# Performance work log

Hardware: AMD Instinct MI355X
Metric: run time of the kernel (lower is better)

The kernel has to match this reference:

```python
import jax, jax.numpy as jnp
import numpy as np

M, K, N = 8192, 4096, 11008
GS = 128
G = K // GS  # 32 groups along reduction dim


def setup_inputs() -> dict:
    key = jax.random.key(0)
    k1, k2, k3, k4 = jax.random.split(key, 4)
    inp = jax.random.normal(k1, (M, K), dtype=jnp.float32)
    # packed int4 weights: two nibbles per byte along K -> [K//2, N]
    weight = jax.random.randint(k2, (K // 2, N), 0, 256, dtype=jnp.int32)
    scale = jax.random.uniform(k3, (G, N), dtype=jnp.float32)
    zp = jax.random.randint(k4, (G, N), 0, 16, dtype=jnp.int32)
    return {"input": inp, "weight": weight, "scale": scale, "zp": zp, "gs": GS}


def dequant_int4(weight, scale, zp, gs):
    # unpack nibbles: low nibble first, then high -> interleaved along K
    low = weight & 0xF            # [K//2, N]
    high = (weight >> 4) & 0xF    # [K//2, N]
    w = jnp.stack([low, high], axis=1).reshape(weight.shape[0] * 2, weight.shape[1])  # [K, N]
    g = w.shape[0] // gs
    wg = w.reshape(g, gs, w.shape[1])                          # [G, gs, N]
    wd = (wg - zp[:, None, :]).astype(scale.dtype) * scale[:, None, :]
    return wd.reshape(w.shape[0], w.shape[1])                  # [K, N] float


def reference(input, weight, scale, zp, gs):
    W = dequant_int4(weight, scale, zp, gs)      # [K, N]
    return input @ W                             # [M, N]
```

## Files before the change

### kernel.cpp

```cpp
#include <hip/hip_runtime.h>


constexpr int M = 8192;
constexpr int K = 4096;
constexpr int N = 11008;

constexpr int BM = 128;
constexpr int BN = 128;
constexpr int BK = 64;

typedef short v8s __attribute__((ext_vector_type(8)));
typedef float v4f __attribute__((ext_vector_type(4)));

__device__ __forceinline__ unsigned pack_bf16(float lo, float hi) {
    unsigned a = __builtin_bit_cast(unsigned, lo);
    a += 0x7FFFu + ((a >> 16) & 1u);
    unsigned b = __builtin_bit_cast(unsigned, hi);
    b += 0x7FFFu + ((b >> 16) & 1u);
    return (a >> 16) | (b & 0xFFFF0000u);
}

__global__ __launch_bounds__(256) void tile_a(const float* __restrict__ A,
                                              uint4* __restrict__ At)
{
    const size_t u = (size_t)blockIdx.x * 256 + threadIdx.x;
    const int r  = (int)(u & 127);
    const int c  = (int)((u >> 7) & 7);
    const int kt = (int)((u >> 10) & 63);
    const int mt = (int)(u >> 16);
    const float* src = A + (size_t)(mt * 128 + r) * K + kt * 64 + c * 8;
    float4 f0 = *reinterpret_cast<const float4*>(src);
    float4 f1 = *reinterpret_cast<const float4*>(src + 4);
    uint4 w;
    w.x = pack_bf16(f0.x, f0.y);
    w.y = pack_bf16(f0.z, f0.w);
    w.z = pack_bf16(f1.x, f1.y);
    w.w = pack_bf16(f1.z, f1.w);
    At[u] = w;
}

__global__ __launch_bounds__(256) void tile_b(const int* __restrict__ Wq,
                                              const float* __restrict__ scale,
                                              const int* __restrict__ zp,
                                              uint4* __restrict__ Bt)
{
    const size_t u = (size_t)blockIdx.x * 256 + threadIdx.x;
    const int r  = (int)(u & 127);
    const int c  = (int)((u >> 7) & 7);
    const int kt = (int)((u >> 10) & 63);
    const int nt = (int)(u >> 16);
    const int n  = nt * 128 + r;
    const int g  = kt >> 1;
    const float sc = scale[(size_t)g * N + n];
    const float zs = -sc * (float)zp[(size_t)g * N + n];
    const int* src = Wq + (size_t)(kt * 32 + c * 4) * N + n;
    unsigned q0 = (unsigned)src[0];
    unsigned q1 = (unsigned)src[(size_t)N];
    unsigned q2 = (unsigned)src[(size_t)2 * N];
    unsigned q3 = (unsigned)src[(size_t)3 * N];
    uint4 o;
    o.x = pack_bf16(fmaf((float)(q0 & 15u), sc, zs),
                    fmaf((float)((q0 >> 4) & 15u), sc, zs));
    o.y = pack_bf16(fmaf((float)(q1 & 15u), sc, zs),
                    fmaf((float)((q1 >> 4) & 15u), sc, zs));
    o.z = pack_bf16(fmaf((float)(q2 & 15u), sc, zs),
                    fmaf((float)((q2 >> 4) & 15u), sc, zs));
    o.w = pack_bf16(fmaf((float)(q3 & 15u), sc, zs),
                    fmaf((float)((q3 >> 4) & 15u), sc, zs));
    Bt[u] = o;
}

__global__ __launch_bounds__(256) void qgemm_bf16(
    const unsigned short* __restrict__ At,
    const unsigned short* __restrict__ Bt,
    float* __restrict__ C)
{
    __shared__ unsigned short sA[(BK / 8) * BM * 8];
    __shared__ unsigned short sB[(BK / 8) * BN * 8];

    const int t = threadIdx.x;

    const int lane = t & 63;
    const int wave = t >> 6;
    const int wm   = (wave & 1) * 64;
    const int wn   = (wave >> 1) * 64;
    const int l16  = lane & 15;
    const int quad = lane >> 4;

    v4f acc[4][4];
    #pragma unroll
    for (int i = 0; i < 4; ++i)
        #pragma unroll
        for (int j = 0; j < 4; ++j)
            acc[i][j] = (v4f){0.f, 0.f, 0.f, 0.f};

    for (int kt = 0; kt < K / BK; ++kt) {
        const unsigned short* aTile = At + ((size_t)(blockIdx.x * 64 + kt) * 1024) * 8;
        const unsigned short* bTile = Bt + ((size_t)(blockIdx.y * 64 + kt) * 1024) * 8;

        __syncthreads();

        #pragma unroll
        for (int i = 0; i < 4; ++i) {
            const int s = i * 256 + t;
            const unsigned short* ga = aTile + (size_t)s * 8;
            const unsigned short* gb = bTile + (size_t)s * 8;
            unsigned short* la = sA + (size_t)(s & ~63) * 8;
            unsigned short* lb = sB + (size_t)(s & ~63) * 8;
            __builtin_amdgcn_global_load_lds(
                (const __attribute__((address_space(1))) void*)ga,
                (__attribute__((address_space(3))) void*)la, 16, 0, 0);
            __builtin_amdgcn_global_load_lds(
                (const __attribute__((address_space(1))) void*)gb,
                (__attribute__((address_space(3))) void*)lb, 16, 0, 0);
        }

        asm volatile("s_waitcnt vmcnt(0)" ::: "memory");
        __syncthreads();

        #pragma unroll
        for (int kw = 0; kw < 2; ++kw) {
            const int cb = kw * 4 + quad;
            v8s af[4], bfr[4];
            #pragma unroll
            for (int i = 0; i < 4; ++i)
                af[i] = *reinterpret_cast<const v8s*>(
                    &sA[(cb * BM + wm + i * 16 + l16) * 8]);
            #pragma unroll
            for (int j = 0; j < 4; ++j)
                bfr[j] = *reinterpret_cast<const v8s*>(
                    &sB[(cb * BN + wn + j * 16 + l16) * 8]);
            #pragma unroll
            for (int i = 0; i < 4; ++i)
                #pragma unroll
                for (int j = 0; j < 4; ++j)
                    acc[i][j] = __builtin_amdgcn_mfma_f32_16x16x32_bf16(
                        af[i], bfr[j], acc[i][j], 0, 0, 0);
        }
    }

    const int m0 = blockIdx.x * BM;
    const int n0 = blockIdx.y * BN;
    #pragma unroll
    for (int i = 0; i < 4; ++i) {
        int rbase = m0 + wm + i * 16 + quad * 4;
        #pragma unroll
        for (int j = 0; j < 4; ++j) {
            int col = n0 + wn + j * 16 + l16;
            #pragma unroll
            for (int r = 0; r < 4; ++r)
                C[(size_t)(rbase + r) * N + col] = acc[i][j][r];
        }
    }
}

__global__ __launch_bounds__(256) void qgemm_kernel(
    const float* __restrict__ A,
    const int*   __restrict__ Wq,
    const float* __restrict__ scale,
    const int*   __restrict__ zp,
    float*       __restrict__ C)
{
    __shared__ unsigned short sA[(BK / 8) * BM * 8];
    __shared__ unsigned short sB[(BK / 8) * BN * 8];

    const int t  = threadIdx.x;
    const int m0 = blockIdx.x * BM;
    const int n0 = blockIdx.y * BN;

    const int lane = t & 63;
    const int wave = t >> 6;
    const int wm   = (wave & 1) * 64;
    const int wn   = (wave >> 1) * 64;
    const int l16  = lane & 15;
    const int quad = lane >> 4;

    const int bn  = t & 127;
    const int brg = t >> 7;

    v4f acc[4][4];
    #pragma unroll
    for (int i = 0; i < 4; ++i)
        #pragma unroll
        for (int j = 0; j < 4; ++j)
            acc[i][j] = (v4f){0.f, 0.f, 0.f, 0.f};

    for (int kt = 0; kt < K / BK; ++kt) {
        const int k0 = kt * BK;
        const int gq = k0 >> 7;
        const float sc = scale[gq * N + n0 + bn];
        const float zs = -sc * (float)zp[gq * N + n0 + bn];

        __syncthreads();

        #pragma unroll
        for (int p = 0; p < 4; ++p) {
            int idx = t + p * 256;
            int m = idx >> 3;
            int c = idx & 7;
            const float* src = A + (size_t)(m0 + m) * K + k0 + c * 8;
            float4 f0 = *reinterpret_cast<const float4*>(src);
            float4 f1 = *reinterpret_cast<const float4*>(src + 4);
            uint4 w;
            w.x = pack_bf16(f0.x, f0.y);
            w.y = pack_bf16(f0.z, f0.w);
            w.z = pack_bf16(f1.x, f1.y);
            w.w = pack_bf16(f1.z, f1.w);
            *reinterpret_cast<uint4*>(&sA[(c * BM + m) * 8]) = w;
        }

        #pragma unroll
        for (int p = 0; p < 4; ++p) {
            int g = brg + p * 2;
            const int* src = Wq + (size_t)((k0 >> 1) + g * 4) * N + n0 + bn;
            unsigned q0 = (unsigned)src[0];
            unsigned q1 = (unsigned)src[N];
            unsigned q2 = (unsigned)src[2 * N];
            unsigned q3 = (unsigned)src[3 * N];
            uint4 o;
            o.x = pack_bf16(fmaf((float)(q0 & 15u), sc, zs),
                            fmaf((float)((q0 >> 4) & 15u), sc, zs));
            o.y = pack_bf16(fmaf((float)(q1 & 15u), sc, zs),
                            fmaf((float)((q1 >> 4) & 15u), sc, zs));
            o.z = pack_bf16(fmaf((float)(q2 & 15u), sc, zs),
                            fmaf((float)((q2 >> 4) & 15u), sc, zs));
            o.w = pack_bf16(fmaf((float)(q3 & 15u), sc, zs),
                            fmaf((float)((q3 >> 4) & 15u), sc, zs));
            *reinterpret_cast<uint4*>(&sB[(g * BN + bn) * 8]) = o;
        }

        __syncthreads();

        #pragma unroll
        for (int kw = 0; kw < 2; ++kw) {
            int cb = kw * 4 + quad;
            v8s af[4], bfr[4];
            #pragma unroll
            for (int i = 0; i < 4; ++i)
                af[i] = *reinterpret_cast<const v8s*>(&sA[(cb * BM + wm + i * 16 + l16) * 8]);
            #pragma unroll
            for (int j = 0; j < 4; ++j)
                bfr[j] = *reinterpret_cast<const v8s*>(&sB[(cb * BN + wn + j * 16 + l16) * 8]);
            #pragma unroll
            for (int i = 0; i < 4; ++i)
                #pragma unroll
                for (int j = 0; j < 4; ++j)
                    acc[i][j] = __builtin_amdgcn_mfma_f32_16x16x32_bf16(
                        af[i], bfr[j], acc[i][j], 0, 0, 0);
        }
    }

    #pragma unroll
    for (int i = 0; i < 4; ++i) {
        int rbase = m0 + wm + i * 16 + quad * 4;
        #pragma unroll
        for (int j = 0; j < 4; ++j) {
            int col = n0 + wn + j * 16 + l16;
            #pragma unroll
            for (int r = 0; r < 4; ++r)
                C[(size_t)(rbase + r) * N + col] = acc[i][j][r];
        }
    }
}

extern "C" void kernel_launch(void* const* d_in, const int* in_sizes, int n_in,
                              void* d_out, int out_size, void* d_ws, size_t ws_size,
                              hipStream_t stream) {
    const float* A     = (const float*)d_in[0];
    const int*   Wq    = (const int*)d_in[1];
    const float* scale = (const float*)d_in[2];
    const int*   zp    = (const int*)d_in[3];
    float*       C     = (float*)d_out;

    const size_t needA = (size_t)M * K * 2;
    const size_t needB = (size_t)(N / 128) * (K / 64) * 1024 * 16;

    if (d_ws != nullptr && ws_size >= needA + needB) {
        unsigned short* At = (unsigned short*)d_ws;
        unsigned short* Bt = (unsigned short*)((char*)d_ws + needA);

        tile_a<<<dim3((unsigned)((size_t)M * K / 8 / 256)), dim3(256), 0, stream>>>(
            A, (uint4*)At);
        tile_b<<<dim3((unsigned)((size_t)(N / 128) * (K / 64) * 1024 / 256)), dim3(256), 0,
                 stream>>>(Wq, scale, zp, (uint4*)Bt);
        qgemm_bf16<<<dim3(M / BM, N / BN), dim3(256), 0, stream>>>(At, Bt, C);
    } else {
        qgemm_kernel<<<dim3(M / BM, N / BN), dim3(256), 0, stream>>>(A, Wq, scale, zp, C);
    }
}
```

Before: 1.268 ms.

## Fuse prep kernels and use 256x256 tiles with 4-stage LDS pipeline

Merges the A-conversion and B-dequant tiling kernels into a single prep launch, rearranged for 256-wide tiles with BK=32. The bf16 GEMM now uses 512-thread blocks computing 256x256 tiles. It keeps three global_load_lds stages in flight across a 4-buffer LDS ring, using partial vmcnt waits, and raises wave priority around the MFMA block. The aim is to hide global-load latency behind compute and raise arithmetic intensity per tile. In exchange it needs 128KB of LDS per block, which limits occupancy to one block per CU, and a larger accumulator register footprint.

```diff
diff --git a/kernel.cpp b/kernel.cpp
--- a/kernel.cpp
+++ b/kernel.cpp
@@ -5,9 +5,10 @@
 constexpr int K = 4096;
 constexpr int N = 11008;
 
-constexpr int BM = 128;
-constexpr int BN = 128;
-constexpr int BK = 64;
+constexpr int BM = 256;
+constexpr int BN = 256;
+constexpr int BK = 32;
+constexpr int KT = K / BK;
 
 typedef short v8s __attribute__((ext_vector_type(8)));
 typedef float v4f __attribute__((ext_vector_type(4)));
@@ -20,65 +21,184 @@
     return (a >> 16) | (b & 0xFFFF0000u);
 }
 
-__global__ __launch_bounds__(256) void tile_a(const float* __restrict__ A,
-                                              uint4* __restrict__ At)
-{
-    const size_t u = (size_t)blockIdx.x * 256 + threadIdx.x;
-    const int r  = (int)(u & 127);
-    const int c  = (int)((u >> 7) & 7);
-    const int kt = (int)((u >> 10) & 63);
-    const int mt = (int)(u >> 16);
-    const float* src = A + (size_t)(mt * 128 + r) * K + kt * 64 + c * 8;
-    float4 f0 = *reinterpret_cast<const float4*>(src);
-    float4 f1 = *reinterpret_cast<const float4*>(src + 4);
-    uint4 w;
-    w.x = pack_bf16(f0.x, f0.y);
-    w.y = pack_bf16(f0.z, f0.w);
-    w.z = pack_bf16(f1.x, f1.y);
-    w.w = pack_bf16(f1.z, f1.w);
-    At[u] = w;
-}
-
-__global__ __launch_bounds__(256) void tile_b(const int* __restrict__ Wq,
-                                              const float* __restrict__ scale,
-                                              const int* __restrict__ zp,
-                                              uint4* __restrict__ Bt)
-{
-    const size_t u = (size_t)blockIdx.x * 256 + threadIdx.x;
-    const int r  = (int)(u & 127);
-    const int c  = (int)((u >> 7) & 7);
-    const int kt = (int)((u >> 10) & 63);
-    const int nt = (int)(u >> 16);
-    const int n  = nt * 128 + r;
-    const int g  = kt >> 1;
-    const float sc = scale[(size_t)g * N + n];
-    const float zs = -sc * (float)zp[(size_t)g * N + n];
-    const int* src = Wq + (size_t)(kt * 32 + c * 4) * N + n;
-    unsigned q0 = (unsigned)src[0];
-    unsigned q1 = (unsigned)src[(size_t)N];
-    unsigned q2 = (unsigned)src[(size_t)2 * N];
-    unsigned q3 = (unsigned)src[(size_t)3 * N];
-    uint4 o;
-    o.x = pack_bf16(fmaf((float)(q0 & 15u), sc, zs),
-                    fmaf((float)((q0 >> 4) & 15u), sc, zs));
-    o.y = pack_bf16(fmaf((float)(q1 & 15u), sc, zs),
-                    fmaf((float)((q1 >> 4) & 15u), sc, zs));
-    o.z = pack_bf16(fmaf((float)(q2 & 15u), sc, zs),
-                    fmaf((float)((q2 >> 4) & 15u), sc, zs));
-    o.w = pack_bf16(fmaf((float)(q3 & 15u), sc, zs),
-                    fmaf((float)((q3 >> 4) & 15u), sc, zs));
-    Bt[u] = o;
-}
-
-__global__ __launch_bounds__(256) void qgemm_bf16(
+constexpr int PREP_A_BLOCKS = (M / 256) * KT * 256 / 256;
+constexpr int PREP_B_BLOCKS = (N / 256) * KT * 4 * 256 / 256;
+
+__global__ __launch_bounds__(256) void prep(const float* __restrict__ A,
+                                            const int* __restrict__ Wq,
+                                            const float* __restrict__ scale,
+                                            const int* __restrict__ zp,
+                                            uint4* __restrict__ At,
+                                            uint4* __restrict__ Bt)
+{
+    const int tid = threadIdx.x;
+    if (blockIdx.x < PREP_A_BLOCKS) {
+        const int u  = blockIdx.x * 256 + tid;
+        const int r  = u & 255;
+        const int kt = (u >> 8) & 127;
+        const int mt = u >> 15;
+        const float* src = A + (size_t)(mt * 256 + r) * K + kt * 32;
+        float4 f[8];
+        #pragma unroll
+        for (int i = 0; i < 8; ++i)
+            f[i] = reinterpret_cast<const float4*>(src)[i];
+        const size_t base = (size_t)(mt * KT + kt) * 1024 + r;
+        #pragma unroll
+        for (int c = 0; c < 4; ++c) {
+            uint4 w;
+            w.x = pack_bf16(f[2 * c].x, f[2 * c].y);
+            w.y = pack_bf16(f[2 * c].z, f[2 * c].w);
+            w.z = pack_bf16(f[2 * c + 1].x, f[2 * c + 1].y);
+            w.w = pack_bf16(f[2 * c + 1].z, f[2 * c + 1].w);
+            At[base + c * 256] = w;
+        }
+    } else {
+        const size_t u = (size_t)(blockIdx.x - PREP_A_BLOCKS) * 256 + tid;
+        const int r  = (int)(u & 255);
+        const int c  = (int)((u >> 8) & 3);
+        const int kt = (int)((u >> 10) & 127);
+        const int nt = (int)(u >> 17);
+        const int n  = nt * 256 + r;
+        const int g  = kt >> 2;
+        const float sc = scale[(size_t)g * N + n];
+        const float zs = -sc * (float)zp[(size_t)g * N + n];
+        const int* src = Wq + (size_t)(kt * 16 + c * 4) * N + n;
+        unsigned q0 = (unsigned)src[0];
+        unsigned q1 = (unsigned)src[(size_t)N];
+        unsigned q2 = (unsigned)src[(size_t)2 * N];
+        unsigned q3 = (unsigned)src[(size_t)3 * N];
+        uint4 o;
+        o.x = pack_bf16(fmaf((float)(q0 & 15u), sc, zs),
+                        fmaf((float)((q0 >> 4) & 15u), sc, zs));
+        o.y = pack_bf16(fmaf((float)(q1 & 15u), sc, zs),
+                        fmaf((float)((q1 >> 4) & 15u), sc, zs));
+        o.z = pack_bf16(fmaf((float)(q2 & 15u), sc, zs),
+                        fmaf((float)((q2 >> 4) & 15u), sc, zs));
+        o.w = pack_bf16(fmaf((float)(q3 & 15u), sc, zs),
+                        fmaf((float)((q3 >> 4) & 15u), sc, zs));
+        Bt[u] = o;
+    }
+}
+
+
+__device__ __forceinline__ void stage_step(const unsigned short* __restrict__ At,
+                                           const unsigned short* __restrict__ Bt,
+                                           int bx, int by, int t, int buf,
+                                           int tid, unsigned short* sMem)
+{
+    const unsigned short* aT = At + (size_t)(bx * KT + t) * 1024 * 8;
+    const unsigned short* bT = Bt + (size_t)(by * KT + t) * 1024 * 8;
+    unsigned short* sa = sMem + (size_t)buf * 2048 * 8;
+    unsigned short* sb = sa + 1024 * 8;
+    #pragma unroll
+    for (int i = 0; i < 2; ++i) {
+        const int s = i * 512 + tid;
+        __builtin_amdgcn_global_load_lds(
+            (const __attribute__((address_space(1))) void*)(aT + (size_t)s * 8),
+            (__attribute__((address_space(3))) void*)(sa + (size_t)(s & ~63) * 8),
+            16, 0, 0);
+        __builtin_amdgcn_global_load_lds(
+            (const __attribute__((address_space(1))) void*)(bT + (size_t)s * 8),
+            (__attribute__((address_space(3))) void*)(sb + (size_t)(s & ~63) * 8),
+            16, 0, 0);
+    }
+}
+
+__device__ __forceinline__ void compute_step(const unsigned short* sMem, int buf,
+                                             int wm, int wn, int quad, int l16,
+                                             v4f (&acc)[8][4])
+{
+    const unsigned short* sa = sMem + (size_t)buf * 2048 * 8;
+    const unsigned short* sb = sa + 1024 * 8;
+    v8s af[8], bfr[4];
+    #pragma unroll
+    for (int i = 0; i < 8; ++i)
+        af[i] = *reinterpret_cast<const v8s*>(&sa[(quad * 256 + wm + i * 16 + l16) * 8]);
+    #pragma unroll
+    for (int j = 0; j < 4; ++j)
+        bfr[j] = *reinterpret_cast<const v8s*>(&sb[(quad * 256 + wn + j * 16 + l16) * 8]);
+    __builtin_amdgcn_s_setprio(1);
+    #pragma unroll
+    for (int i = 0; i < 8; ++i)
+        #pragma unroll
+        for (int j = 0; j < 4; ++j)
+            acc[i][j] = __builtin_amdgcn_mfma_f32_16x16x32_bf16(
+                af[i], bfr[j], acc[i][j], 0, 0, 0);
+    __builtin_amdgcn_s_setprio(0);
+}
+
+__global__ __launch_bounds__(512, 2) void qgemm_bf16(
     const unsigned short* __restrict__ At,
     const unsigned short* __restrict__ Bt,
     float* __restrict__ C)
 {
-    __shared__ unsigned short sA[(BK / 8) * BM * 8];
-    __shared__ unsigned short sB[(BK / 8) * BN * 8];
-
-    const int t = threadIdx.x;
+    __shared__ unsigned short sMem[4 * 2048 * 8];
+
+    const int tid  = threadIdx.x;
+    const int bx   = blockIdx.x;
+    const int by   = blockIdx.y;
+    const int lane = tid & 63;
+    const int wave = tid >> 6;
+    const int wm   = (wave >> 2) * 128;
+    const int wn   = (wave & 3) * 64;
+    const int l16  = lane & 15;
+    const int quad = lane >> 4;
+
+    v4f acc[8][4];
+    #pragma unroll
+    for (int i = 0; i < 8; ++i)
+        #pragma unroll
+        for (int j = 0; j < 4; ++j)
+            acc[i][j] = (v4f){0.f, 0.f, 0.f, 0.f};
+
+    stage_step(At, Bt, bx, by, 0, 0, tid, sMem);
+    stage_step(At, Bt, bx, by, 1, 1, tid, sMem);
+    stage_step(At, Bt, bx, by, 2, 2, tid, sMem);
+
+    for (int t = 0; t < KT; ++t) {
+        if (t < KT - 2) {
+            asm volatile("s_waitcnt vmcnt(8)" ::: "memory");
+        } else if (t == KT - 2) {
+            asm volatile("s_waitcnt vmcnt(4)" ::: "memory");
+        } else {
+            asm volatile("s_waitcnt vmcnt(0)" ::: "memory");
+        }
+        __builtin_amdgcn_s_barrier();
+        if (t + 3 < KT)
+            stage_step(At, Bt, bx, by, t + 3, (t + 3) & 3, tid, sMem);
+        compute_step(sMem, t & 3, wm, wn, quad, l16, acc);
+    }
+
+    const int m0 = bx * BM;
+    const int n0 = by * BN;
+    #pragma unroll
+    for (int i = 0; i < 8; ++i) {
+        int rbase = m0 + wm + i * 16 + quad * 4;
+        #pragma unroll
+        for (int j = 0; j < 4; ++j) {
+            int col = n0 + wn + j * 16 + l16;
+            #pragma unroll
+            for (int r = 0; r < 4; ++r)
+                C[(size_t)(rbase + r) * N + col] = acc[i][j][r];
+        }
+    }
+}
+
+constexpr int FBM = 128, FBN = 128, FBK = 64;
+
+__global__ __launch_bounds__(256) void qgemm_kernel(
+    const float* __restrict__ A,
+    const int*   __restrict__ Wq,
+    const float* __restrict__ scale,
+    const int*   __restrict__ zp,
+    float*       __restrict__ C)
+{
+    __shared__ unsigned short sA[(FBK / 8) * FBM * 8];
+    __shared__ unsigned short sB[(FBK / 8) * FBN * 8];
+
+    const int t  = threadIdx.x;
+    const int m0 = blockIdx.x * FBM;
+    const int n0 = blockIdx.y * FBN;
 
     const int lane = t & 63;
     const int wave = t >> 6;
@@ -87,6 +207,9 @@
     const int l16  = lane & 15;
     const int quad = lane >> 4;
 
+    const int bn  = t & 127;
+    const int brg = t >> 7;
+
     v4f acc[4][4];
     #pragma unroll
     for (int i = 0; i < 4; ++i)
@@ -94,99 +217,8 @@
         for (int j = 0; j < 4; ++j)
             acc[i][j] = (v4f){0.f, 0.f, 0.f, 0.f};
 
-    for (int kt = 0; kt < K / BK; ++kt) {
-        const unsigned short* aTile = At + ((size_t)(blockIdx.x * 64 + kt) * 1024) * 8;
-        const unsigned short* bTile = Bt + ((size_t)(blockIdx.y * 64 + kt) * 1024) * 8;
-
-        __syncthreads();
-
-        #pragma unroll
-        for (int i = 0; i < 4; ++i) {
-            const int s = i * 256 + t;
-            const unsigned short* ga = aTile + (size_t)s * 8;
-            const unsigned short* gb = bTile + (size_t)s * 8;
-            unsigned short* la = sA + (size_t)(s & ~63) * 8;
-            unsigned short* lb = sB + (size_t)(s & ~63) * 8;
-            __builtin_amdgcn_global_load_lds(
-                (const __attribute__((address_space(1))) void*)ga,
-                (__attribute__((address_space(3))) void*)la, 16, 0, 0);
-            __builtin_amdgcn_global_load_lds(
-                (const __attribute__((address_space(1))) void*)gb,
-                (__attribute__((address_space(3))) void*)lb, 16, 0, 0);
-        }
-
-        asm volatile("s_waitcnt vmcnt(0)" ::: "memory");
-        __syncthreads();
-
-        #pragma unroll
-        for (int kw = 0; kw < 2; ++kw) {
-            const int cb = kw * 4 + quad;
-            v8s af[4], bfr[4];
-            #pragma unroll
-            for (int i = 0; i < 4; ++i)
-                af[i] = *reinterpret_cast<const v8s*>(
-                    &sA[(cb * BM + wm + i * 16 + l16) * 8]);
-            #pragma unroll
-            for (int j = 0; j < 4; ++j)
-                bfr[j] = *reinterpret_cast<const v8s*>(
-                    &sB[(cb * BN + wn + j * 16 + l16) * 8]);
-            #pragma unroll
-            for (int i = 0; i < 4; ++i)
-                #pragma unroll
-                for (int j = 0; j < 4; ++j)
-                    acc[i][j] = __builtin_amdgcn_mfma_f32_16x16x32_bf16(
-                        af[i], bfr[j], acc[i][j], 0, 0, 0);
-        }
-    }
-
-    const int m0 = blockIdx.x * BM;
-    const int n0 = blockIdx.y * BN;
-    #pragma unroll
-    for (int i = 0; i < 4; ++i) {
-        int rbase = m0 + wm + i * 16 + quad * 4;
-        #pragma unroll
-        for (int j = 0; j < 4; ++j) {
-            int col = n0 + wn + j * 16 + l16;
-            #pragma unroll
-            for (int r = 0; r < 4; ++r)
-                C[(size_t)(rbase + r) * N + col] = acc[i][j][r];
-        }
-    }
-}
-
-__global__ __launch_bounds__(256) void qgemm_kernel(
-    const float* __restrict__ A,
-    const int*   __restrict__ Wq,
-    const float* __restrict__ scale,
-    const int*   __restrict__ zp,
-    float*       __restrict__ C)
-{
-    __shared__ unsigned short sA[(BK / 8) * BM * 8];
-    __shared__ unsigned short sB[(BK / 8) * BN * 8];
-
-    const int t  = threadIdx.x;
-    const int m0 = blockIdx.x * BM;
-    const int n0 = blockIdx.y * BN;
-
-    const int lane = t & 63;
-    const int wave = t >> 6;
-    const int wm   = (wave & 1) * 64;
-    const int wn   = (wave >> 1) * 64;
-    const int l16  = lane & 15;
-    const int quad = lane >> 4;
-
-    const int bn  = t & 127;
-    const int brg = t >> 7;
-
-    v4f acc[4][4];
-    #pragma unroll
-    for (int i = 0; i < 4; ++i)
-        #pragma unroll
-        for (int j = 0; j < 4; ++j)
-            acc[i][j] = (v4f){0.f, 0.f, 0.f, 0.f};
-
-    for (int kt = 0; kt < K / BK; ++kt) {
-        const int k0 = kt * BK;
+    for (int kt = 0; kt < K / FBK; ++kt) {
+        const int k0 = kt * FBK;
         const int gq = k0 >> 7;
         const float sc = scale[gq * N + n0 + bn];
         const float zs = -sc * (float)zp[gq * N + n0 + bn];
@@ -206,7 +238,7 @@
             w.y = pack_bf16(f0.z, f0.w);
             w.z = pack_bf16(f1.x, f1.y);
             w.w = pack_bf16(f1.z, f1.w);
-            *reinterpret_cast<uint4*>(&sA[(c * BM + m) * 8]) = w;
+            *reinterpret_cast<uint4*>(&sA[(c * FBM + m) * 8]) = w;
         }
 
         #pragma unroll
@@ -226,7 +258,7 @@
                             fmaf((float)((q2 >> 4) & 15u), sc, zs));
             o.w = pack_bf16(fmaf((float)(q3 & 15u), sc, zs),
                             fmaf((float)((q3 >> 4) & 15u), sc, zs));
-            *reinterpret_cast<uint4*>(&sB[(g * BN + bn) * 8]) = o;
+            *reinterpret_cast<uint4*>(&sB[(g * FBN + bn) * 8]) = o;
         }
 
         __syncthreads();
@@ -237,10 +269,10 @@
             v8s af[4], bfr[4];
             #pragma unroll
             for (int i = 0; i < 4; ++i)
-                af[i] = *reinterpret_cast<const v8s*>(&sA[(cb * BM + wm + i * 16 + l16) * 8]);
+                af[i] = *reinterpret_cast<const v8s*>(&sA[(cb * FBM + wm + i * 16 + l16) * 8]);
             #pragma unroll
             for (int j = 0; j < 4; ++j)
-                bfr[j] = *reinterpret_cast<const v8s*>(&sB[(cb * BN + wn + j * 16 + l16) * 8]);
+                bfr[j] = *reinterpret_cast<const v8s*>(&sB[(cb * FBN + wn + j * 16 + l16) * 8]);
             #pragma unroll
             for (int i = 0; i < 4; ++i)
                 #pragma unroll
@@ -273,18 +305,16 @@
     float*       C     = (float*)d_out;
 
     const size_t needA = (size_t)M * K * 2;
-    const size_t needB = (size_t)(N / 128) * (K / 64) * 1024 * 16;
+    const size_t needB = (size_t)N * K * 2;
 
     if (d_ws != nullptr && ws_size >= needA + needB) {
         unsigned short* At = (unsigned short*)d_ws;
         unsigned short* Bt = (unsigned short*)((char*)d_ws + needA);
 
-        tile_a<<<dim3((unsigned)((size_t)M * K / 8 / 256)), dim3(256), 0, stream>>>(
-            A, (uint4*)At);
-        tile_b<<<dim3((unsigned)((size_t)(N / 128) * (K / 64) * 1024 / 256)), dim3(256), 0,
-                 stream>>>(Wq, scale, zp, (uint4*)Bt);
-        qgemm_bf16<<<dim3(M / BM, N / BN), dim3(256), 0, stream>>>(At, Bt, C);
+        prep<<<dim3(PREP_A_BLOCKS + PREP_B_BLOCKS), dim3(256), 0, stream>>>(
+            A, Wq, scale, zp, (uint4*)At, (uint4*)Bt);
+        qgemm_bf16<<<dim3(M / BM, N / BN), dim3(512), 0, stream>>>(At, Bt, C);
     } else {
-        qgemm_kernel<<<dim3(M / BM, N / BN), dim3(256), 0, stream>>>(A, Wq, scale, zp, C);
-    }
-}
+        qgemm_kernel<<<dim3(M / FBM, N / FBN), dim3(256), 0, stream>>>(A, Wq, scale, zp, C);
+    }
+}
```

New measurement: 1.148 ms. 1.11x faster.
